# Performance work log

Measured on AMD Instinct MI355X. Metric: run time of the kernel, lower is better.

## Reference

```python
import jax, jax.numpy as jnp
import numpy as np

K_ACTIVE = 32
MULTI_K = 64
AUX_K = 64
DEAD_THRESH = 256


def setup_inputs() -> dict:
    key = jax.random.key(0)
    ks = jax.random.split(key, 4)
    B, D, M = 4096, 1024, 16384
    x = jax.random.normal(ks[0], (B, D), dtype=jnp.float32)
    enc_w = jax.random.normal(ks[1], (M, D), dtype=jnp.float32) / np.sqrt(D)
    dec_w = jax.random.normal(ks[2], (D, M), dtype=jnp.float32) / np.sqrt(M)
    input_bias = jnp.zeros((D,), dtype=jnp.float32)
    neuron_bias = jnp.zeros((M,), dtype=jnp.float32)
    steps = jax.random.randint(ks[3], (M,), 0, 512).astype(jnp.int64)
    return {"x": x, "enc_w": enc_w, "dec_w": dec_w,
            "input_bias": input_bias, "neuron_bias": neuron_bias, "steps": steps}


def reference(x, enc_w, dec_w, input_bias, neuron_bias, steps):
    # encode: center, linear (no bias), add neuron bias, relu
    x_cent = x - input_bias                                   # [B, D]
    pre_act = x_cent @ enc_w.T + neuron_bias                  # [B, M]
    acts = jax.nn.relu(pre_act)
    B, M = acts.shape

    # training path: global batch-wide top-(K*B) across flattened activations
    flat = acts.reshape(-1)                                   # [B*M]
    topk_vals, topk_idx = jax.lax.top_k(flat, K_ACTIVE * B)
    activ = jnp.zeros_like(flat).at[topk_idx].set(topk_vals).reshape(B, M)

    # multi-k branch: per-row top-k on pre-activations, relu, scatter, decode
    mvals, midx = jax.lax.top_k(pre_act, MULTI_K)             # [B, MULTI_K]
    mvals = jax.nn.relu(mvals)
    rows = jnp.arange(B)[:, None]
    multik_activ = jnp.zeros_like(pre_act).at[rows, midx].set(mvals)
    multik_recon = multik_activ @ dec_w.T + input_bias        # [B, D]

    # main reconstruction
    recon = activ @ dec_w.T + input_bias                      # [B, D]

    # dead-neuron bookkeeping + aux top-k over dead neurons
    steps = steps + 1
    active = activ.sum(axis=0) > 0                            # [M]
    steps = jnp.where(active, jnp.zeros_like(steps), steps)
    dead_mask = (steps > DEAD_THRESH).astype(pre_act.dtype)   # [M]
    dead_pre = pre_act * dead_mask                            # [B, M]
    aux_vals, aux_idx = jax.lax.top_k(dead_pre, AUX_K)        # [B, AUX_K]
    aux_vals = jax.nn.relu(aux_vals)

    return recon, activ, multik_recon, aux_vals, aux_idx
```

## Files before the change

### kernel.cpp

```cpp
#include <hip/hip_runtime.h>

#define K_ACTIVE 32
#define MULTI_K 64
#define AUX_K 64
#define DEAD_THRESH 256
#define BUF_CAP 2097152u
#define STG_CAP 4096
#define SORT_CAP 4096

typedef unsigned int u32;
typedef unsigned long long u64;
typedef unsigned short ushort_t;
typedef __bf16 bf16x8 __attribute__((ext_vector_type(8)));
typedef float f32x4 __attribute__((ext_vector_type(4)));

__device__ __forceinline__ u32 fmap_signed_bits(u32 u) {
  return (u & 0x80000000u) ? ~u : (u | 0x80000000u);
}

__device__ __forceinline__ u32 bf16_rne(float f) {
  u32 u = __float_as_uint(f);
  return (u + 0x7FFFu + ((u >> 16) & 1u)) >> 16;
}

__device__ __forceinline__ void gload16(const void* g, void* s) {
  __builtin_amdgcn_global_load_lds(
      (const __attribute__((address_space(1))) void*)g,
      (__attribute__((address_space(3))) void*)s, 16, 0, 0);
}

__global__ void transpose_k(const float* __restrict__ in, float* __restrict__ out, int D, int M) {
  __shared__ float tile[32][33];
  const int bx = blockIdx.x * 32;
  const int by = blockIdx.y * 32;
  const int tx = threadIdx.x, ty = threadIdx.y;
  #pragma unroll
  for (int i = 0; i < 32; i += 8)
    tile[ty + i][tx] = in[(size_t)(by + ty + i) * M + bx + tx];
  __syncthreads();
  #pragma unroll
  for (int i = 0; i < 32; i += 8)
    out[(size_t)(bx + ty + i) * D + by + tx] = tile[tx][ty + i];
}

__global__ void convA_k(const float* __restrict__ X, const float* __restrict__ IB,
                        ushort_t* __restrict__ AH, ushort_t* __restrict__ AL, int D) {
  const int idx = blockIdx.x * 256 + threadIdx.x;
  const int row = idx >> 7;
  const int dpos = (idx & 127) << 3;
  const float4* xr = reinterpret_cast<const float4*>(X + (size_t)row * D + dpos);
  const float4* br = reinterpret_cast<const float4*>(IB + dpos);
  float4 x0 = xr[0], x1 = xr[1], b0 = br[0], b1 = br[1];
  float c[8] = {x0.x - b0.x, x0.y - b0.y, x0.z - b0.z, x0.w - b0.w,
                x1.x - b1.x, x1.y - b1.y, x1.z - b1.z, x1.w - b1.w};
  u32 hw[4], lw[4];
  #pragma unroll
  for (int j = 0; j < 4; ++j) {
    u32 h0 = bf16_rne(c[2 * j]), h1 = bf16_rne(c[2 * j + 1]);
    float r0 = c[2 * j] - __uint_as_float(h0 << 16);
    float r1 = c[2 * j + 1] - __uint_as_float(h1 << 16);
    hw[j] = h0 | (h1 << 16);
    lw[j] = bf16_rne(r0) | (bf16_rne(r1) << 16);
  }
  reinterpret_cast<uint4*>(AH)[idx] = make_uint4(hw[0], hw[1], hw[2], hw[3]);
  reinterpret_cast<uint4*>(AL)[idx] = make_uint4(lw[0], lw[1], lw[2], lw[3]);
}

__global__ void convW_k(const float* __restrict__ W,
                        ushort_t* __restrict__ WH, ushort_t* __restrict__ WL) {
  const int idx = blockIdx.x * 256 + threadIdx.x;
  const float4* wr = reinterpret_cast<const float4*>(W) + (size_t)idx * 2;
  float4 x0 = wr[0], x1 = wr[1];
  float c[8] = {x0.x, x0.y, x0.z, x0.w, x1.x, x1.y, x1.z, x1.w};
  u32 hw[4], lw[4];
  #pragma unroll
  for (int j = 0; j < 4; ++j) {
    u32 h0 = bf16_rne(c[2 * j]), h1 = bf16_rne(c[2 * j + 1]);
    float r0 = c[2 * j] - __uint_as_float(h0 << 16);
    float r1 = c[2 * j + 1] - __uint_as_float(h1 << 16);
    hw[j] = h0 | (h1 << 16);
    lw[j] = bf16_rne(r0) | (bf16_rne(r1) << 16);
  }
  reinterpret_cast<uint4*>(WH)[idx] = make_uint4(hw[0], hw[1], hw[2], hw[3]);
  reinterpret_cast<uint4*>(WL)[idx] = make_uint4(lw[0], lw[1], lw[2], lw[3]);
}

__global__ __launch_bounds__(256) void gemm_mfma(
    const ushort_t* __restrict__ AH, const ushort_t* __restrict__ AL,
    const ushort_t* __restrict__ WH, const ushort_t* __restrict__ WL,
    const float* __restrict__ NB, float* __restrict__ OUT,
    u32* __restrict__ GH, u32* __restrict__ CM, int M) {
  extern __shared__ char smem[];
  ushort_t* sA = (ushort_t*)smem;
  ushort_t* sB = (ushort_t*)(smem + 16384);
  const int tid = threadIdx.x;
  const int wave = tid >> 6, lane = tid & 63;
  const int bm = blockIdx.y * 128, bn = blockIdx.x * 128;
  const int wm = wave & 1, wn = wave >> 1;

  f32x4 acc[4][4];
  #pragma unroll
  for (int i = 0; i < 4; ++i)
    #pragma unroll
    for (int j = 0; j < 4; ++j) acc[i][j] = (f32x4){0.f, 0.f, 0.f, 0.f};

  int rowA[4], cbS[4];
  #pragma unroll
  for (int r = 0; r < 4; ++r) {
    int o = ((wave << 2) + r) * 1024 + lane * 16;
    int row = o >> 7;
    int cb = o & 127;
    rowA[r] = row;
    cbS[r] = cb ^ ((row & 7) << 4);
  }
  const int cl = lane & 15, kg = lane >> 4;

  for (int kt = 0; kt < 48; ++kt) {
    const int ph = kt >> 4;
    const size_t kb = (size_t)((kt & 15) << 6) * 2;
    const ushort_t* Asrc = (ph == 1) ? AL : AH;
    const ushort_t* Bsrc = (ph == 2) ? WL : WH;
    #pragma unroll
    for (int r = 0; r < 4; ++r) {
      gload16((const char*)Asrc + ((size_t)(bm + rowA[r]) * 2048 + kb + cbS[r]),
              (char*)sA + (((wave << 2) + r) << 10));
      gload16((const char*)Bsrc + ((size_t)(bn + rowA[r]) * 2048 + kb + cbS[r]),
              (char*)sB + (((wave << 2) + r) << 10));
    }
    __syncthreads();
    #pragma unroll
    for (int ks = 0; ks < 2; ++ks) {
      const int kbyte = ks * 64 + kg * 16;
      bf16x8 af[4], bfr[4];
      #pragma unroll
      for (int mi = 0; mi < 4; ++mi) {
        const int rA = wm * 64 + mi * 16 + cl;
        af[mi] = *reinterpret_cast<const bf16x8*>(
            (const char*)sA + rA * 128 + (kbyte ^ ((rA & 7) << 4)));
      }
      #pragma unroll
      for (int ni = 0; ni < 4; ++ni) {
        const int rB = wn * 64 + ni * 16 + cl;
        bfr[ni] = *reinterpret_cast<const bf16x8*>(
            (const char*)sB + rB * 128 + (kbyte ^ ((rB & 7) << 4)));
      }
      #pragma unroll
      for (int mi = 0; mi < 4; ++mi)
        #pragma unroll
        for (int ni = 0; ni < 4; ++ni)
          acc[mi][ni] = __builtin_amdgcn_mfma_f32_16x16x32_bf16(af[mi], bfr[ni], acc[mi][ni], 0, 0, 0);
    }
    __syncthreads();
  }

  u32* eh = (u32*)smem;
  for (int i = tid; i < 8192; i += 256) eh[i] = 0;
  __syncthreads();
  const int rg = lane >> 4;
  const int rb = (lane & 3) * 2048;
  #pragma unroll
  for (int ni = 0; ni < 4; ++ni) {
    const int col = bn + wn * 64 + ni * 16 + cl;
    const float nbv = NB[col];
    float mx = 0.f;
    #pragma unroll
    for (int mi = 0; mi < 4; ++mi) {
      const int row0 = bm + wm * 64 + mi * 16 + rg * 4;
      #pragma unroll
      for (int r = 0; r < 4; ++r) {
        const float val = acc[mi][ni][r] + nbv;
        OUT[(size_t)(row0 + r) * M + col] = val;
        const float a = (val > 0.f) ? val : 0.f;
        mx = fmaxf(mx, a);
        atomicAdd(&eh[rb + (__float_as_uint(a) >> 21)], 1u);
      }
    }
    mx = fmaxf(mx, __shfl_xor(mx, 16));
    mx = fmaxf(mx, __shfl_xor(mx, 32));
    if (rg == 0) atomicMax(&CM[col], __float_as_uint(mx));
  }
  __syncthreads();
  for (int i = tid; i < 2048; i += 256) {
    u32 s = eh[i] + eh[2048 + i] + eh[4096 + i] + eh[6144 + i];
    if (s) atomicAdd(&GH[i], s);
  }
}

__global__ void scan_k(const u32* __restrict__ H, u32* __restrict__ PRM, u32 K, int phase) {
  __shared__ u32 suf[256];
  const int t = threadIdx.x;
  u32 h[8], ls[8];
  #pragma unroll
  for (int j = 0; j < 8; ++j) h[j] = H[t * 8 + j];
  u32 run = 0;
  #pragma unroll
  for (int j = 7; j >= 0; --j) { run += h[j]; ls[j] = run; }
  suf[t] = run;
  __syncthreads();
  for (int off = 1; off < 256; off <<= 1) {
    u32 v = (t + off < 256) ? suf[t + off] : 0u;
    __syncthreads();
    suf[t] += v;
    __syncthreads();
  }
  const u32 rightOf = (t < 255) ? suf[t + 1] : 0u;
  const u32 base = (phase == 2) ? PRM[1] : 0u;
  #pragma unroll
  for (int j = 0; j < 8; ++j) {
    u32 Sb = base + rightOf + ls[j];
    u32 Sb1 = base + rightOf + ((j < 7) ? ls[j + 1] : 0u);
    if (Sb >= K && Sb1 < K) {
      int b = t * 8 + j;
      if (phase == 1) { PRM[0] = (u32)b; PRM[1] = Sb1; }
      else { PRM[2] = (PRM[0] << 11) | (u32)b; PRM[3] = K - Sb1; }
    }
  }
}

__global__ void hist2_k(const float4* __restrict__ P4, size_t N4, u32* __restrict__ PRM,
                        u32* __restrict__ GH, float* __restrict__ BV, u32* __restrict__ BI) {
  __shared__ float sv[STG_CAP];
  __shared__ u32 si[STG_CAP];
  __shared__ u32 scnt, sbase;
  const int tid = threadIdx.x;
  if (tid == 0) scnt = 0;
  __syncthreads();
  const u32 b1 = PRM[0];
  const size_t step = (size_t)gridDim.x * blockDim.x;
  for (size_t i = (size_t)blockIdx.x * blockDim.x + tid; i < N4; i += step) {
    float4 vv = P4[i];
    float va[4] = {vv.x, vv.y, vv.z, vv.w};
    #pragma unroll
    for (int c = 0; c < 4; ++c) {
      float a = (va[c] > 0.f) ? va[c] : 0.f;
      u32 u = __float_as_uint(a);
      if ((u >> 21) == b1) {
        atomicAdd(&GH[(u >> 10) & 2047u], 1u);
        u32 p = atomicAdd(&scnt, 1u);
        if (p < STG_CAP) { sv[p] = a; si[p] = (u32)(i * 4 + c); }
        else {
          u32 g = atomicAdd(&PRM[8], 1u);
          if (g < BUF_CAP) { BV[g] = a; BI[g] = (u32)(i * 4 + c); }
        }
      }
    }
  }
  __syncthreads();
  u32 n = scnt < STG_CAP ? scnt : STG_CAP;
  if (tid == 0) sbase = atomicAdd(&PRM[8], n);
  __syncthreads();
  const u32 base = sbase;
  for (u32 i = tid; i < n; i += 256) {
    u32 g = base + i;
    if (g < BUF_CAP) { BV[g] = sv[i]; BI[g] = si[i]; }
  }
}

__global__ void collect2_k(u32* __restrict__ PRM, const float* __restrict__ BV,
                           const u32* __restrict__ BI, float* __restrict__ BV2,
                           u32* __restrict__ BI2) {
  const u32 pc = PRM[2];
  u32 nb1 = PRM[8]; if (nb1 > BUF_CAP) nb1 = BUF_CAP;
  const u32 step = gridDim.x * blockDim.x;
  for (u32 i = blockIdx.x * blockDim.x + threadIdx.x; i < nb1; i += step) {
    float a = BV[i];
    if ((__float_as_uint(a) >> 10) == pc) {
      u32 pos = atomicAdd(&PRM[9], 1u);
      if (pos < SORT_CAP) { BV2[pos] = a; BI2[pos] = BI[i]; }
    }
  }
}

__global__ void sortmark_k(u32* __restrict__ PRM, const float* __restrict__ BV, const u32* __restrict__ BI,
                           float* __restrict__ SV, u32* __restrict__ SI, u32* __restrict__ CF, int M) {
  __shared__ u64 keys[SORT_CAP];
  const int tid = threadIdx.x;
  u32 nb = PRM[9]; if (nb > SORT_CAP) nb = SORT_CAP;
  const u32 krem = PRM[3];
  if (nb == 0) { if (tid == 0) PRM[5] = 0; return; }
  u32 np = 1; while (np < nb) np <<= 1;
  for (u32 i = tid; i < np; i += 256)
    keys[i] = (i < nb) ? ((((u64)__float_as_uint(BV[i])) << 32) | (u64)(0xFFFFFFFFu - BI[i])) : 0ull;
  __syncthreads();
  for (u32 k = 2; k <= np; k <<= 1) {
    for (u32 j = k >> 1; j > 0; j >>= 1) {
      for (u32 i = tid; i < np; i += 256) {
        u32 ixj = i ^ j;
        if (ixj > i) {
          u64 a = keys[i], b = keys[ixj];
          bool up = ((i & k) == 0);
          if (up ? (a < b) : (a > b)) { keys[i] = b; keys[ixj] = a; }
        }
      }
      __syncthreads();
    }
  }
  u32 nsel = krem < nb ? krem : nb;
  for (u32 t = tid; t < nsel; t += 256) {
    u64 kk = keys[t];
    u32 flat = 0xFFFFFFFFu - (u32)(kk & 0xFFFFFFFFull);
    float val = __uint_as_float((u32)(kk >> 32));
    SI[t] = flat; SV[t] = val;
    if (val > 0.f) CF[flat % (u32)M] = 1u;
  }
  if (tid == 0) PRM[5] = nsel;
}

__global__ void dead_k(const u32* __restrict__ CF, const u32* __restrict__ CM,
                       const int* __restrict__ ST, const u32* __restrict__ PRM,
                       u32* __restrict__ DW, int M) {
  int w = blockIdx.x * blockDim.x + threadIdx.x;
  if (w >= M / 32) return;
  const u32 pc = PRM[2];
  u32 bits = 0;
  for (int i = 0; i < 32; ++i) {
    int n = w * 32 + i;
    bool active = (CF[n] != 0) || ((CM[n] >> 10) > pc);
    if (!active && (ST[n] + 1) > DEAD_THRESH) bits |= (1u << i);
  }
  DW[w] = bits;
}

struct TopkSh {
  u32 hist[16 * 257];
  u32 wred[4];
  u32 prefix, need, scnt;
  int selN[64];
  float selV[64];
};

template<bool ZSKIP>
__device__ __forceinline__ void row_topk64(const float (&v)[64], int tid, TopkSh* S) {
  const int lane = tid & 63, wid = tid >> 6;
  u32 zp = 0, zn = 0;
  if (ZSKIP) {
    #pragma unroll
    for (int j = 0; j < 64; ++j) {
      u32 ub = __float_as_uint(v[j]);
      zp += (ub == 0u);
      zn += (ub == 0x80000000u);
    }
    #pragma unroll
    for (int o = 32; o > 0; o >>= 1) { zp += __shfl_down(zp, o); zn += __shfl_down(zn, o); }
  }
  u32 pref = 0, need = 64;
  for (int p = 0; p < 4; ++p) {
    const int sh = 24 - 8 * p;
    for (int i = tid; i < 16 * 257; i += 256) S->hist[i] = 0;
    if (p == 0 && tid == 0) S->scnt = 0;
    __syncthreads();
    const int rb = (tid & 15) * 257;
    #pragma unroll
    for (int j = 0; j < 64; ++j) {
      u32 ub = __float_as_uint(v[j]);
      if (ZSKIP && ((ub << 1) == 0u)) continue;
      u32 mu = fmap_signed_bits(ub);
      if (p == 0 || (mu >> (sh + 8)) == pref)
        atomicAdd(&S->hist[rb + ((mu >> sh) & 255u)], 1u);
    }
    if (ZSKIP && lane == 0) {
      const u32 mup = 0x80000000u, mun = 0x7FFFFFFFu;
      if (zp && (p == 0 || (mup >> (sh + 8)) == pref))
        atomicAdd(&S->hist[wid * 257 + ((mup >> sh) & 255u)], zp);
      if (zn && (p == 0 || (mun >> (sh + 8)) == pref))
        atomicAdd(&S->hist[wid * 257 + ((mun >> sh) & 255u)], zn);
    }
    __syncthreads();
    u32 own = 0;
    #pragma unroll
    for (int r = 0; r < 16; ++r) own += S->hist[r * 257 + tid];
    u32 x = own;
    #pragma unroll
    for (int o = 1; o < 64; o <<= 1) {
      u32 y = __shfl_down(x, o);
      x += (lane + o < 64) ? y : 0u;
    }
    if (lane == 0) S->wred[wid] = x;
    __syncthreads();
    u32 Sb = x;
    for (int w = wid + 1; w < 4; ++w) Sb += S->wred[w];
    u32 below = Sb - own;
    if (Sb >= need && below < need) {
      S->prefix = (pref << 8) | (u32)tid;
      S->need = need - below;
    }
    __syncthreads();
    pref = S->prefix; need = S->need;
  }
  const u32 muc = pref, neq = need;
  u32 myeq = 0;
  #pragma unroll
  for (int j = 0; j < 64; ++j) {
    u32 mu = fmap_signed_bits(__float_as_uint(v[j]));
    if (mu > muc) {
      u32 pos = atomicAdd(&S->scnt, 1u);
      S->selN[pos] = tid * 64 + j;
      S->selV[pos] = v[j];
    } else if (mu == muc) ++myeq;
  }
  u32 xs = myeq;
  #pragma unroll
  for (int o = 1; o < 64; o <<= 1) {
    u32 y = __shfl_up(xs, o);
    xs += (lane >= o) ? y : 0u;
  }
  if (lane == 63) S->wred[wid] = xs;
  __syncthreads();
  u32 base = 0;
  for (int w = 0; w < wid; ++w) base += S->wred[w];
  u32 g = base + xs - myeq;
  const u32 a0 = S->scnt;
  #pragma unroll
  for (int j = 0; j < 64; ++j) {
    u32 mu = fmap_signed_bits(__float_as_uint(v[j]));
    if (mu == muc) {
      if (g < neq) { S->selN[a0 + g] = tid * 64 + j; S->selV[a0 + g] = v[j]; }
      ++g;
    }
  }
  __syncthreads();
}

__device__ __forceinline__ void load_row64(const float* rowp, float (&v)[64]) {
  #pragma unroll
  for (int j = 0; j < 16; ++j) {
    float4 t = reinterpret_cast<const float4*>(rowp)[j];
    v[4 * j + 0] = t.x; v[4 * j + 1] = t.y; v[4 * j + 2] = t.z; v[4 * j + 3] = t.w;
  }
}

__launch_bounds__(256, 2)
__global__ void rowk_multik(const float* __restrict__ PRE, const float* __restrict__ WT,
                            const float* __restrict__ IB, float* __restrict__ MR,
                            int M, int D) {
  __shared__ TopkSh S;
  const int b = blockIdx.x, tid = threadIdx.x;
  float v[64];
  load_row64(PRE + (size_t)b * M + tid * 64, v);
  row_topk64<false>(v, tid, &S);
  const int d0 = tid * 4;
  float4 acc = *reinterpret_cast<const float4*>(IB + d0);
  for (int i = 0; i < 64; ++i) {
    float w = S.selV[i];
    if (w > 0.f) {
      const float4 wv = *reinterpret_cast<const float4*>(WT + (size_t)S.selN[i] * D + d0);
      acc.x = fmaf(w, wv.x, acc.x); acc.y = fmaf(w, wv.y, acc.y);
      acc.z = fmaf(w, wv.z, acc.z); acc.w = fmaf(w, wv.w, acc.w);
    }
  }
  *reinterpret_cast<float4*>(MR + (size_t)b * D + d0) = acc;
}

__launch_bounds__(256, 2)
__global__ void rowk_aux(const float* __restrict__ PRE, const u32* __restrict__ DW,
                         float* __restrict__ AV, float* __restrict__ AI, int M) {
  __shared__ TopkSh S;
  __shared__ u64 skey[64];
  __shared__ int sN2[64];
  __shared__ float sV2[64];
  const int b = blockIdx.x, tid = threadIdx.x;
  float v[64];
  load_row64(PRE + (size_t)b * M + tid * 64, v);
  const u32 mw0 = DW[tid * 2], mw1 = DW[tid * 2 + 1];
  #pragma unroll
  for (int j = 0; j < 64; ++j) {
    u32 bit = ((j < 32 ? mw0 : mw1) >> (j & 31)) & 1u;
    v[j] = bit ? v[j] : (v[j] * 0.0f);
  }
  row_topk64<true>(v, tid, &S);
  if (tid < 64) {
    float vv = S.selV[tid];
    int col = S.selN[tid];
    u32 mu = fmap_signed_bits(__float_as_uint(vv));
    skey[tid] = (((u64)mu) << 32) | (u64)(0xFFFFFFFFu - (u32)col);
  }
  __syncthreads();
  if (tid < 64) {
    u64 mine = skey[tid];
    int rank = 0;
    for (int j = 0; j < 64; ++j) rank += (skey[j] > mine) ? 1 : 0;
    sN2[rank] = S.selN[tid]; sV2[rank] = S.selV[tid];
  }
  __syncthreads();
  if (tid < 64) {
    AV[(size_t)b * AUX_K + tid] = sV2[tid] > 0.f ? sV2[tid] : 0.f;
    AI[(size_t)b * AUX_K + tid] = (float)sN2[tid];
  }
}

__launch_bounds__(256, 2)
__global__ void rowk_scatter(float* __restrict__ ACT, const float* __restrict__ WT,
                             const float* __restrict__ IB, float* __restrict__ RC,
                             const u32* __restrict__ PRM, const float* __restrict__ SV,
                             const u32* __restrict__ SI, int M, int D) {
  __shared__ int lsN[2048]; __shared__ float lsV[2048];
  __shared__ int ovN[256]; __shared__ float ovV[256];
  __shared__ u32 ovc, lc;
  const int b = blockIdx.x, tid = threadIdx.x;
  float* rowp = ACT + (size_t)b * M + tid * 64;
  float v[64];
  load_row64(rowp, v);
  const u32 pc = PRM[2];
  #pragma unroll
  for (int j = 0; j < 64; ++j) {
    float a = (v[j] > 0.f) ? v[j] : 0.f;
    v[j] = ((__float_as_uint(a) >> 10) > pc) ? a : 0.f;
  }
  if (tid == 0) ovc = 0;
  __syncthreads();
  const u32 nbs = PRM[5];
  for (u32 t = tid; t < nbs; t += 256) {
    u32 flat = SI[t];
    if (flat / (u32)M == (u32)b) {
      u32 p = atomicAdd(&ovc, 1u);
      if (p < 256) { ovN[p] = (int)(flat % (u32)M); ovV[p] = SV[t]; }
    }
  }
  __syncthreads();
  const u32 no = ovc < 256u ? ovc : 256u;
  #pragma unroll
  for (int j = 0; j < 64; ++j) {
    const int col = tid * 64 + j;
    for (u32 i = 0; i < no; ++i) if (ovN[i] == col) v[j] = ovV[i];
  }
  #pragma unroll
  for (int j = 0; j < 16; ++j) {
    float4 t = make_float4(v[4 * j + 0], v[4 * j + 1], v[4 * j + 2], v[4 * j + 3]);
    reinterpret_cast<float4*>(rowp)[j] = t;
  }
  const int d0 = tid * 4;
  float4 acc = *reinterpret_cast<const float4*>(IB + d0);
  for (int cpart = 0; cpart < 8; ++cpart) {
    if (tid == 0) lc = 0;
    __syncthreads();
    if ((tid >> 5) == cpart) {
      #pragma unroll
      for (int j = 0; j < 64; ++j) {
        if (v[j] > 0.f) {
          u32 p = atomicAdd(&lc, 1u);
          lsN[p] = tid * 64 + j; lsV[p] = v[j];
        }
      }
    }
    __syncthreads();
    const u32 n = lc;
    for (u32 i = 0; i < n; ++i) {
      const float w = lsV[i];
      const float4 wv = *reinterpret_cast<const float4*>(WT + (size_t)lsN[i] * D + d0);
      acc.x = fmaf(w, wv.x, acc.x); acc.y = fmaf(w, wv.y, acc.y);
      acc.z = fmaf(w, wv.z, acc.z); acc.w = fmaf(w, wv.w, acc.w);
    }
    __syncthreads();
  }
  *reinterpret_cast<float4*>(RC + (size_t)b * D + d0) = acc;
}

extern "C" void kernel_launch(void* const* d_in, const int* in_sizes, int n_in,
                              void* d_out, int out_size, void* d_ws, size_t ws_size,
                              hipStream_t stream) {
  const float* x  = (const float*)d_in[0];
  const float* ew = (const float*)d_in[1];
  const float* dw = (const float*)d_in[2];
  const float* ib = (const float*)d_in[3];
  const float* nb = (const float*)d_in[4];
  const int* steps = (const int*)d_in[5];
  const int D = in_sizes[3];
  const int M = in_sizes[4];
  const int B = in_sizes[0] / D;
  const u32 K = (u32)(K_ACTIVE * B);

  float* out = (float*)d_out;
  float* recon  = out;
  float* activ  = out + (size_t)B * D;
  float* mrecon = activ + (size_t)B * M;
  float* avals  = mrecon + (size_t)B * D;
  float* aidx   = avals + (size_t)B * AUX_K;

  ushort_t* AH = (ushort_t*)recon;
  ushort_t* AL = (ushort_t*)mrecon;

  char* wsp = (char*)d_ws;
  size_t o = 0;
  auto alloc = [&](size_t bytes) { char* p = wsp + o; o += (bytes + 255) & ~(size_t)255; return p; };
  ushort_t* WH = (ushort_t*)alloc((size_t)M * D * 2);
  ushort_t* WL = (ushort_t*)alloc((size_t)M * D * 2);
  float* WT = (float*)alloc((size_t)M * D * 4);
  u32* H1   = (u32*)alloc(8192);
  u32* H2   = (u32*)alloc(8192);
  u32* PRM  = (u32*)alloc(256);
  u32* CF   = (u32*)alloc((size_t)M * 4);
  u32* CM   = (u32*)alloc((size_t)M * 4);
  u32* DW   = (u32*)alloc((size_t)(M / 32) * 4);
  float* BV = (float*)alloc((size_t)BUF_CAP * 4);
  u32* BI   = (u32*)alloc((size_t)BUF_CAP * 4);
  float* BV2 = (float*)alloc((size_t)SORT_CAP * 4);
  u32* BI2   = (u32*)alloc((size_t)SORT_CAP * 4);
  float* SV = (float*)alloc((size_t)SORT_CAP * 4);
  u32* SI   = (u32*)alloc((size_t)SORT_CAP * 4);
  (void)ws_size; (void)n_in; (void)out_size;

  hipMemsetAsync(H1, 0, 8192, stream);
  hipMemsetAsync(H2, 0, 8192, stream);
  hipMemsetAsync(PRM, 0, 256, stream);
  hipMemsetAsync(CF, 0, (size_t)M * 4, stream);
  hipMemsetAsync(CM, 0, (size_t)M * 4, stream);

  convA_k<<<(B * D / 8 + 255) / 256, 256, 0, stream>>>(x, ib, AH, AL, D);
  convW_k<<<((size_t)M * D / 8 + 255) / 256, 256, 0, stream>>>(ew, WH, WL);
  transpose_k<<<dim3(M / 32, D / 32), dim3(32, 8), 0, stream>>>(dw, WT, D, M);
  gemm_mfma<<<dim3(M / 128, B / 128), 256, 32768, stream>>>(AH, AL, WH, WL, nb, activ, H1, CM, M);

  const size_t N4 = (size_t)B * M / 4;
  const float4* act4 = (const float4*)activ;
  scan_k<<<1, 256, 0, stream>>>(H1, PRM, K, 1);
  hist2_k<<<2048, 256, 0, stream>>>(act4, N4, PRM, H2, BV, BI);
  scan_k<<<1, 256, 0, stream>>>(H2, PRM, K, 2);
  collect2_k<<<64, 256, 0, stream>>>(PRM, BV, BI, BV2, BI2);
  sortmark_k<<<1, 256, 0, stream>>>(PRM, BV2, BI2, SV, SI, CF, M);
  dead_k<<<(M / 32 + 255) / 256, 256, 0, stream>>>(CF, CM, steps, PRM, DW, M);
  rowk_multik<<<B, 256, 0, stream>>>(activ, WT, ib, mrecon, M, D);
  rowk_aux<<<B, 256, 0, stream>>>(activ, DW, avals, aidx, M);
  rowk_scatter<<<B, 256, 0, stream>>>(activ, WT, ib, recon, PRM, SV, SI, M, D);
}
```

Baseline: 1.492 ms.

## Collect top-k candidates in GEMM epilogue to skip full second-pass scan

The GEMM epilogue now stages every activation of at least 2.0 in shared memory and appends it, with its flat index, to the global candidate buffer. When the first-pass threshold bin is at or above the bin for 2.0, a new small kernel builds the second-level histogram from that buffer alone. Otherwise the original full scan of the activation matrix still runs as a fallback. This removes a full read of the large activation array in the common case. The cost is extra shared atomics and global writes in the epilogue, a dependence on the buffer capacity, and one extra kernel launch.

Result: slower. 2.393 ms (+60.4%).

```diff
diff --git a/kernel.cpp b/kernel.cpp
--- a/kernel.cpp
+++ b/kernel.cpp
@@ -6,7 +6,9 @@
 #define DEAD_THRESH 256
 #define BUF_CAP 2097152u
 #define STG_CAP 4096
+#define CAND_CAP 1024
 #define SORT_CAP 4096
+#define SAFE_BIN 0x200u
 
 typedef unsigned int u32;
 typedef unsigned long long u64;
@@ -89,10 +91,14 @@
     const ushort_t* __restrict__ AH, const ushort_t* __restrict__ AL,
     const ushort_t* __restrict__ WH, const ushort_t* __restrict__ WL,
     const float* __restrict__ NB, float* __restrict__ OUT,
-    u32* __restrict__ GH, u32* __restrict__ CM, int M) {
+    u32* __restrict__ GH, u32* __restrict__ CM,
+    float* __restrict__ BV, u32* __restrict__ BI, u32* __restrict__ PRM, int M) {
   extern __shared__ char smem[];
   ushort_t* sA = (ushort_t*)smem;
   ushort_t* sB = (ushort_t*)(smem + 16384);
+  __shared__ float cv[CAND_CAP];
+  __shared__ u32 ci[CAND_CAP];
+  __shared__ u32 ccnt, cbase;
   const int tid = threadIdx.x;
   const int wave = tid >> 6, lane = tid & 63;
   const int bm = blockIdx.y * 128, bn = blockIdx.x * 128;
@@ -155,6 +161,7 @@
 
   u32* eh = (u32*)smem;
   for (int i = tid; i < 8192; i += 256) eh[i] = 0;
+  if (tid == 0) ccnt = 0;
   __syncthreads();
   const int rg = lane >> 4;
   const int rb = (lane & 3) * 2048;
@@ -173,6 +180,15 @@
         const float a = (val > 0.f) ? val : 0.f;
         mx = fmaxf(mx, a);
         atomicAdd(&eh[rb + (__float_as_uint(a) >> 21)], 1u);
+        if (a >= 2.0f) {
+          u32 p = atomicAdd(&ccnt, 1u);
+          u32 flat = (u32)(row0 + r) * (u32)M + (u32)col;
+          if (p < CAND_CAP) { cv[p] = a; ci[p] = flat; }
+          else {
+            u32 g = atomicAdd(&PRM[8], 1u);
+            if (g < BUF_CAP) { BV[g] = a; BI[g] = flat; }
+          }
+        }
       }
     }
     mx = fmaxf(mx, __shfl_xor(mx, 16));
@@ -183,6 +199,14 @@
   for (int i = tid; i < 2048; i += 256) {
     u32 s = eh[i] + eh[2048 + i] + eh[4096 + i] + eh[6144 + i];
     if (s) atomicAdd(&GH[i], s);
+  }
+  u32 n = ccnt < CAND_CAP ? ccnt : CAND_CAP;
+  if (tid == 0) cbase = atomicAdd(&PRM[8], n);
+  __syncthreads();
+  const u32 base = cbase;
+  for (u32 i = tid; i < n; i += 256) {
+    u32 g = base + i;
+    if (g < BUF_CAP) { BV[g] = cv[i]; BI[g] = ci[i]; }
   }
 }
 
@@ -217,15 +241,28 @@
   }
 }
 
-__global__ void hist2_k(const float4* __restrict__ P4, size_t N4, u32* __restrict__ PRM,
-                        u32* __restrict__ GH, float* __restrict__ BV, u32* __restrict__ BI) {
+__global__ void hist2c_k(const u32* __restrict__ PRM, const float* __restrict__ BV,
+                         u32* __restrict__ GH) {
+  const u32 b1 = PRM[0];
+  if (b1 < SAFE_BIN) return;
+  u32 n = PRM[8]; if (n > BUF_CAP) n = BUF_CAP;
+  const u32 step = gridDim.x * blockDim.x;
+  for (u32 i = blockIdx.x * blockDim.x + threadIdx.x; i < n; i += step) {
+    u32 u = __float_as_uint(BV[i]);
+    if ((u >> 21) == b1) atomicAdd(&GH[(u >> 10) & 2047u], 1u);
+  }
+}
+
+__global__ void hist2f_k(const float4* __restrict__ P4, size_t N4, u32* __restrict__ PRM,
+                         u32* __restrict__ GH, float* __restrict__ BV, u32* __restrict__ BI) {
+  const u32 b1 = PRM[0];
+  if (b1 >= SAFE_BIN) return;
   __shared__ float sv[STG_CAP];
   __shared__ u32 si[STG_CAP];
   __shared__ u32 scnt, sbase;
   const int tid = threadIdx.x;
   if (tid == 0) scnt = 0;
   __syncthreads();
-  const u32 b1 = PRM[0];
   const size_t step = (size_t)gridDim.x * blockDim.x;
   for (size_t i = (size_t)blockIdx.x * blockDim.x + tid; i < N4; i += step) {
     float4 vv = P4[i];
@@ -608,12 +645,14 @@
   convA_k<<<(B * D / 8 + 255) / 256, 256, 0, stream>>>(x, ib, AH, AL, D);
   convW_k<<<((size_t)M * D / 8 + 255) / 256, 256, 0, stream>>>(ew, WH, WL);
   transpose_k<<<dim3(M / 32, D / 32), dim3(32, 8), 0, stream>>>(dw, WT, D, M);
-  gemm_mfma<<<dim3(M / 128, B / 128), 256, 32768, stream>>>(AH, AL, WH, WL, nb, activ, H1, CM, M);
+  gemm_mfma<<<dim3(M / 128, B / 128), 256, 32768, stream>>>(AH, AL, WH, WL, nb, activ,
+                                                            H1, CM, BV, BI, PRM, M);
 
   const size_t N4 = (size_t)B * M / 4;
   const float4* act4 = (const float4*)activ;
   scan_k<<<1, 256, 0, stream>>>(H1, PRM, K, 1);
-  hist2_k<<<2048, 256, 0, stream>>>(act4, N4, PRM, H2, BV, BI);
+  hist2c_k<<<1024, 256, 0, stream>>>(PRM, BV, H2);
+  hist2f_k<<<2048, 256, 0, stream>>>(act4, N4, PRM, H2, BV, BI);
   scan_k<<<1, 256, 0, stream>>>(H2, PRM, K, 2);
   collect2_k<<<64, 256, 0, stream>>>(PRM, BV, BI, BV2, BI2);
   sortmark_k<<<1, 256, 0, stream>>>(PRM, BV2, BI2, SV, SI, CF, M);
```
